# Kernel optimization log

Measured on AMD Instinct MI355X. Metric: run time of the kernel, lower is better.

Reference implementation:

```python
import jax, jax.numpy as jnp
import numpy as np

VOCAB = 64
EMB = 128
H = 256
OUT = 1
NUM_IN = 7
NUM_OUT = 4
B = 64
S = 2048
D_IN = EMB + NUM_OUT  # input_dim to the 1x1 convs


def setup_inputs() -> dict:
    key = jax.random.key(0)
    ks = jax.random.split(key, 12)
    ev = jax.random.randint(ks[0], (B, S, 1), 0, VOCAB).astype(jnp.float32)
    num = jax.random.normal(ks[1], (B, S, NUM_IN), dtype=jnp.float32)
    X = jnp.concatenate([ev, num], axis=-1)  # [B,S,1+NUM_IN]
    sc = lambda fan_in: 1.0 / np.sqrt(fan_in)
    return {
        "X": X,
        "emb": jax.random.normal(ks[2], (VOCAB, EMB), dtype=jnp.float32),
        "num_W": jax.random.normal(ks[3], (NUM_IN, NUM_OUT), dtype=jnp.float32) * sc(NUM_IN),
        "num_b": jnp.zeros((NUM_OUT,), jnp.float32),
        "Wf": jax.random.normal(ks[4], (D_IN, 3 * H), dtype=jnp.float32) * sc(D_IN),
        "bf": jnp.zeros((3 * H,), jnp.float32),
        "Wb": jax.random.normal(ks[5], (D_IN, 3 * H), dtype=jnp.float32) * sc(D_IN),
        "bb": jnp.zeros((3 * H,), jnp.float32),
        "Mu": jax.random.normal(ks[6], (2 * H, 1), dtype=jnp.float32) * sc(2 * H),
        "out_W": jax.random.normal(ks[7], (2 * H, OUT), dtype=jnp.float32) * sc(2 * H),
        "out_b": jnp.zeros((OUT,), jnp.float32),
    }


def _fo_pool(conv_out):
    # conv_out: [B, S, 3H] (already time-ordered as desired). Returns [B, S, H]
    Z, F, O = jnp.split(conv_out, 3, axis=-1)  # O computed but unused (as in source)
    Z = jnp.tanh(Z)
    F = jax.nn.sigmoid(F)
    # scan over time with state [B, H]
    Zt = jnp.swapaxes(Z, 0, 1)  # [S,B,H]
    Ft = jnp.swapaxes(F, 0, 1)
    h0 = jnp.zeros(Z.shape[::2][:1] + Z.shape[2:], Z.dtype) if False else jnp.zeros((Z.shape[0], Z.shape[2]), Z.dtype)
    def step(h, zf):
        z, f = zf
        h = f * h + (1.0 - f) * z
        return h, h
    _, hs = jax.lax.scan(step, h0, (Zt, Ft))  # [S,B,H] in scan order
    return jnp.swapaxes(hs, 0, 1)  # [B,S,H]


def reference(X, emb, num_W, num_b, Wf, bf, Wb, bb, Mu, out_W, out_b):
    ev = X[:, :, 0].astype(jnp.int32)            # event ids
    num = X[:, :, 1:]                             # numeric features [B,S,7]
    e = emb[ev]                                   # [B,S,EMB]
    n = num @ num_W + num_b                       # [B,S,NUM_OUT]
    x = jnp.concatenate([e, n], axis=-1)          # [B,S,D_IN]
    cf = x @ Wf + bf                              # 1x1 conv == pointwise linear, [B,S,3H]
    cb = x @ Wb + bb
    h_fwd = _fo_pool(cf)                          # [B,S,H], time order
    # backward direction: source iterates t = S-1..0 and stacks in append order
    h_bwd = _fo_pool(cb[:, ::-1, :])              # [B,S,H], reversed-time order (faithful)
    hc = jnp.concatenate([h_fwd, h_bwd], axis=-1) # [B,S,2H]
    scores = hc @ Mu                              # [B,S,1]
    w = jax.nn.softmax(scores, axis=1)
    ctx = jnp.sum(hc * w, axis=1)                 # [B,2H]
    return ctx @ out_W + out_b                    # [B,OUT]
```

## Files before the change

kernel.cpp:

```cpp
#include <hip/hip_runtime.h>
#include <stdint.h>

#define VOCABN 64
#define EMBN   128
#define HDIM   256
#define NUMIN  7
#define BN     64
#define SN     2048
#define TWOH   512
#define SEG    16
#define SEGLEN 128

#define CZ 2.8853900818f
#define CF 1.4426950409f

__device__ __forceinline__ float rcpf(float x){ return __builtin_amdgcn_rcpf(x); }

__device__ __forceinline__ float fast_exp2(float x){
#if __has_builtin(__builtin_amdgcn_exp2f)
    return __builtin_amdgcn_exp2f(x);
#else
    return exp2f(x);
#endif
}

__device__ __forceinline__ float2 pk_fma_s_lo(uint64_t a, float2 b, float2 c){
    float2 d;
    asm("v_pk_fma_f32 %0, %1, %2, %3 op_sel_hi:[0,1,1]" : "=v"(d) : "s"(a), "v"(b), "v"(c));
    return d;
}
__device__ __forceinline__ float2 pk_fma_s_hi(uint64_t a, float2 b, float2 c){
    float2 d;
    asm("v_pk_fma_f32 %0, %1, %2, %3 op_sel:[1,0,0] op_sel_hi:[1,1,1]" : "=v"(d) : "s"(a), "v"(b), "v"(c));
    return d;
}

__device__ __forceinline__ uint32_t cvt_pk_bf16(float a, float b){
    uint32_t r;
    asm("v_cvt_pk_bf16_f32 %0, %1, %2" : "=v"(r) : "v"(a), "v"(b));
    return r;
}

__device__ __forceinline__ float waveRedDpp(float x){
    x += __int_as_float(__builtin_amdgcn_update_dpp(0, __float_as_int(x), 0x111, 0xf, 0xf, false));
    x += __int_as_float(__builtin_amdgcn_update_dpp(0, __float_as_int(x), 0x112, 0xf, 0xf, false));
    x += __int_as_float(__builtin_amdgcn_update_dpp(0, __float_as_int(x), 0x114, 0xf, 0xf, false));
    x += __int_as_float(__builtin_amdgcn_update_dpp(0, __float_as_int(x), 0x118, 0xf, 0xf, false));
    x += __int_as_float(__builtin_amdgcn_update_dpp(0, __float_as_int(x), 0x142, 0xa, 0xf, false));
    x += __int_as_float(__builtin_amdgcn_update_dpp(0, __float_as_int(x), 0x143, 0xc, 0xf, false));
    return x;
}

__global__ __launch_bounds__(256) void k0_prep(const float* __restrict__ X, float* __restrict__ Xp)
{
    const int r = blockIdx.x*256 + threadIdx.x;
    const float4* src = (const float4*)(X + (size_t)r*8);
    const float4 a = src[0], b4 = src[1];
    float4* dst = (float4*)(Xp + (size_t)r*8);
    dst[0] = make_float4(a.y, a.z, a.w, b4.x);
    dst[1] = make_float4(b4.y, b4.z, b4.w, __int_as_float((int)a.x * (HDIM*8)));
}

__global__ __launch_bounds__(512) void k1_tables(
    const float* __restrict__ emb, const float* __restrict__ num_W, const float* __restrict__ num_b,
    const float* __restrict__ Wf, const float* __restrict__ bf,
    const float* __restrict__ Wb, const float* __restrict__ bb,
    float* __restrict__ T, float* __restrict__ U)
{
    const int blk = blockIdx.x;
    const int c = threadIdx.x;
    const int j = c & (HDIM-1);
    const int g = c >> 8;
    const int col = g*HDIM + j;
    const float gs = g ? CF : CZ;
    if (blk < 2*VOCABN) {
        const int dir = blk & 1, v = blk >> 1;
        const float* W    = dir ? Wb : Wf;
        const float* bias = dir ? bb : bf;
        float acc = bias[col];
        const float* e = emb + (size_t)v*EMBN;
        #pragma unroll 8
        for (int k=0;k<EMBN;++k) acc = fmaf(e[k], W[(size_t)k*768 + col], acc);
        #pragma unroll
        for (int m=0;m<4;++m)    acc = fmaf(num_b[m], W[(size_t)(EMBN+m)*768 + col], acc);
        T[(((size_t)dir*VOCABN + v)*HDIM + j)*2 + g] = acc * gs;
    } else {
        const int dir = blk - 2*VOCABN;
        const float* W = dir ? Wb : Wf;
        #pragma unroll
        for (int i=0;i<NUMIN;++i){
            float acc = 0.f;
            #pragma unroll
            for (int m=0;m<4;++m) acc = fmaf(num_W[i*4+m], W[(size_t)(EMBN+m)*768 + col], acc);
            U[(((size_t)dir*8 + i)*HDIM + j)*2 + g] = acc * gs;
        }
    }
}

template<int MODE>
__global__ __launch_bounds__(128) void k2_scan(
    const float* __restrict__ Xp, const float* __restrict__ T, const float* __restrict__ U,
    const float* __restrict__ Mu, const float* __restrict__ w,
    const float* __restrict__ hstart,
    float* __restrict__ aArr, float* __restrict__ cArr,
    float* __restrict__ swp, float* __restrict__ ctxp, uint32_t* __restrict__ h2)
{
    const int bid = blockIdx.x;
    const int seg = bid & (SEG-1);
    const int dir = (bid >> 4) & 1;
    const int b   = bid >> 5;
    const int j   = threadIdx.x;
    const int blk = (b*2+dir)*SEG + seg;
    const size_t segIdx = (size_t)blk*HDIM + j;

    const float2* Td2 = (const float2*)T + (size_t)dir*VOCABN*HDIM;
    const float2* Ud2 = (const float2*)U + (size_t)dir*8*HDIM;
    float2 uLo0=Ud2[0*HDIM+j],     uLo1=Ud2[1*HDIM+j],     uLo2=Ud2[2*HDIM+j],
           uLo3=Ud2[3*HDIM+j],     uLo4=Ud2[4*HDIM+j],     uLo5=Ud2[5*HDIM+j],
           uLo6=Ud2[6*HDIM+j];
    float2 uHi0=Ud2[0*HDIM+j+128], uHi1=Ud2[1*HDIM+j+128], uHi2=Ud2[2*HDIM+j+128],
           uHi3=Ud2[3*HDIM+j+128], uHi4=Ud2[4*HDIM+j+128], uHi5=Ud2[5*HDIM+j+128],
           uHi6=Ud2[6*HDIM+j+128];
    const float muLo = (MODE==1 || MODE==3) ? Mu[dir*HDIM + j]       : 0.f;
    const float muHi = (MODE==1 || MODE==3) ? Mu[dir*HDIM + j + 128] : 0.f;

    const int sBeg = seg*SEGLEN;
    const int r0   = b*SN + (dir ? (SN-1-sBeg) : sBeg);
    const int dstep= dir ? -1 : 1;
    const uint64_t* xq = (const uint64_t*)Xp;
    const float* wb = w + (size_t)b*SN + sBeg;
    const char* Tb = (const char*)Td2;
    const int j8 = j*8;

    #define ROWQ(si,k) (xq[(size_t)(r0 + dstep*(si))*4 + (k)])
    #define TROW(q)    (Tb + (int)((q)>>32))

    uint64_t qa0=ROWQ(0,0), qa1=ROWQ(0,1), qa2=ROWQ(0,2), qa3=ROWQ(0,3);
    uint64_t qb0=ROWQ(1,0), qb1=ROWQ(1,1), qb2=ROWQ(1,2), qb3=ROWQ(1,3);
    uint64_t qc0=ROWQ(2,0), qc1=ROWQ(2,1), qc2=ROWQ(2,2), qc3=ROWQ(2,3);
    uint64_t qd0=ROWQ(3,0), qd1=ROWQ(3,1), qd2=ROWQ(3,2), qd3=ROWQ(3,3);
    const char* tp0 = TROW(qa3);
    const char* tp1 = TROW(qb3);
    float2 tLo0 = *(const float2*)(tp0 + j8);
    float2 tHi0 = *(const float2*)(tp0 + j8 + 1024);
    float2 tLo1 = *(const float2*)(tp1 + j8);
    float2 tHi1 = *(const float2*)(tp1 + j8 + 1024);

    float hLo = (MODE==0) ? 0.f : hstart[segIdx];
    float hHi = (MODE==0) ? 0.f : hstart[segIdx + 128];
    float aaccLo = 1.f, aaccHi = 1.f;
    float ctxLo = 0.f, ctxHi = 0.f;
    float hpLo = 0.f, hpHi = 0.f;
    float* swpp = swp + (size_t)(b*4 + dir*2 + (j>>6))*SN + sBeg;
    uint32_t* h2p = h2 + (size_t)blk*(SEGLEN/2)*HDIM + j;

    #pragma unroll 4
    for (int si=0; si<SEGLEN; ++si){
        const int i4 = (si+4 < SEGLEN) ? si+4 : SEGLEN-1;
        const uint64_t qe0=ROWQ(i4,0), qe1=ROWQ(i4,1), qe2=ROWQ(i4,2), qe3=ROWQ(i4,3);
        const char* tp2 = TROW(qc3);
        const float2 tLo2 = *(const float2*)(tp2 + j8);
        const float2 tHi2 = *(const float2*)(tp2 + j8 + 1024);

        float2 zfLo = tLo0, zfHi = tHi0;
        zfLo = pk_fma_s_lo(qa0, uLo0, zfLo);  zfHi = pk_fma_s_lo(qa0, uHi0, zfHi);
        zfLo = pk_fma_s_hi(qa0, uLo1, zfLo);  zfHi = pk_fma_s_hi(qa0, uHi1, zfHi);
        zfLo = pk_fma_s_lo(qa1, uLo2, zfLo);  zfHi = pk_fma_s_lo(qa1, uHi2, zfHi);
        zfLo = pk_fma_s_hi(qa1, uLo3, zfLo);  zfHi = pk_fma_s_hi(qa1, uHi3, zfHi);
        zfLo = pk_fma_s_lo(qa2, uLo4, zfLo);  zfHi = pk_fma_s_lo(qa2, uHi4, zfHi);
        zfLo = pk_fma_s_hi(qa2, uLo5, zfLo);  zfHi = pk_fma_s_hi(qa2, uHi5, zfHi);
        zfLo = pk_fma_s_lo(qa3, uLo6, zfLo);  zfHi = pk_fma_s_lo(qa3, uHi6, zfHi);

        const float e2zL = fast_exp2(zfLo.x), efL = fast_exp2(zfLo.y);
        const float e2zH = fast_exp2(zfHi.x), efH = fast_exp2(zfHi.y);
        const float a2L = 1.f + e2zL, a1L = 1.f + efL;
        const float a2H = 1.f + e2zH, a1H = 1.f + efH;
        const float rL = rcpf(a1L * a2L);
        const float rH = rcpf(a1H * a2H);
        hLo = fmaf(efL * hLo, a2L, e2zL - 1.f) * rL;
        hHi = fmaf(efH * hHi, a2H, e2zH - 1.f) * rH;

        if (MODE==0){
            aaccLo *= efL * a2L * rL;
            aaccHi *= efH * a2H * rH;
        } else if (MODE==1 || MODE==3){
            float pr = waveRedDpp(fmaf(hHi, muHi, hLo * muLo));
            if ((j & 63) == 63) swpp[si] = pr;
            if (MODE==1){
                if (si & 1){
                    h2p[0]   = cvt_pk_bf16(hpLo, hLo);
                    h2p[128] = cvt_pk_bf16(hpHi, hHi);
                    h2p += HDIM;
                } else { hpLo = hLo; hpHi = hHi; }
            }
        } else {
            const float ws_ = wb[si];
            ctxLo = fmaf(ws_, hLo, ctxLo);
            ctxHi = fmaf(ws_, hHi, ctxHi);
        }
        qa0=qb0; qa1=qb1; qa2=qb2; qa3=qb3;
        qb0=qc0; qb1=qc1; qb2=qc2; qb3=qc3;
        qc0=qd0; qc1=qd1; qc2=qd2; qc3=qd3;
        qd0=qe0; qd1=qe1; qd2=qe2; qd3=qe3;
        tLo0=tLo1; tHi0=tHi1; tLo1=tLo2; tHi1=tHi2;
    }
    #undef ROWQ
    #undef TROW
    if (MODE==0){
        aArr[segIdx] = aaccLo; aArr[segIdx+128] = aaccHi;
        cArr[segIdx] = hLo;    cArr[segIdx+128] = hHi;
    }
    if (MODE==2){ ctxp[segIdx] = ctxLo; ctxp[segIdx+128] = ctxHi; }
}

__global__ __launch_bounds__(256) void k_compose(const float* __restrict__ aArr, const float* __restrict__ cArr,
                                                 float* __restrict__ hstart)
{
    const int bd = blockIdx.x;
    const int j  = threadIdx.x;
    float h = 0.f;
    #pragma unroll
    for (int seg=0; seg<SEG; ++seg){
        const size_t idx = ((size_t)bd*SEG + seg)*HDIM + j;
        hstart[idx] = h;
        h = fmaf(aArr[idx], h, cArr[idx]);
    }
}

__global__ __launch_bounds__(256) void k3_softmax(const float* __restrict__ swp, float* __restrict__ w)
{
    __shared__ float sc[SN];
    __shared__ float red[4];
    const int b = blockIdx.x, t = threadIdx.x;
    for (int s=t; s<SN; s+=256){
        float acc = 0.f;
        #pragma unroll
        for (int r=0;r<4;++r) acc += swp[((size_t)b*4 + r)*SN + s];
        sc[s] = acc;
    }
    __syncthreads();
    float m = -3.4e38f;
    for (int s=t; s<SN; s+=256) m = fmaxf(m, sc[s]);
    #pragma unroll
    for (int o=32;o;o>>=1) m = fmaxf(m, __shfl_xor(m,o,64));
    if ((t&63)==0) red[t>>6] = m;
    __syncthreads();
    m = fmaxf(fmaxf(red[0],red[1]), fmaxf(red[2],red[3]));
    float zs = 0.f;
    for (int s=t; s<SN; s+=256){
        float e = __expf(sc[s]-m);
        sc[s] = e;
        zs += e;
    }
    #pragma unroll
    for (int o=32;o;o>>=1) zs += __shfl_xor(zs,o,64);
    __syncthreads();
    if ((t&63)==0) red[t>>6] = zs;
    __syncthreads();
    zs = red[0]+red[1]+red[2]+red[3];
    float invz = rcpf(zs);
    for (int s=t; s<SN; s+=256) w[(size_t)b*SN + s] = sc[s]*invz;
}

__global__ __launch_bounds__(256) void k4_ctx(const uint32_t* __restrict__ h2, const float* __restrict__ w,
                                              float* __restrict__ ctxp)
{
    const int bid = blockIdx.x;
    const int seg = bid & (SEG-1);
    const int dir = (bid >> 4) & 1;
    const int b   = bid >> 5;
    const int blk = (b*2+dir)*SEG + seg;
    const int j   = threadIdx.x;
    const float* wb = w + (size_t)b*SN + seg*SEGLEN;
    const uint32_t* hp = h2 + (size_t)blk*(SEGLEN/2)*HDIM + j;
    float acc = 0.f;
    #pragma unroll 8
    for (int si2=0; si2<SEGLEN/2; ++si2){
        const uint32_t pk = hp[(size_t)si2*HDIM];
        const float hlo = __int_as_float(pk << 16);
        const float hhi = __int_as_float(pk & 0xffff0000u);
        acc = fmaf(wb[2*si2  ], hlo, acc);
        acc = fmaf(wb[2*si2+1], hhi, acc);
    }
    ctxp[(size_t)blk*HDIM + j] = acc;
}

__global__ __launch_bounds__(512) void k5_out(const float* __restrict__ ctxp, const float* __restrict__ out_W,
                                              const float* __restrict__ out_b, float* __restrict__ out)
{
    __shared__ float red[8];
    const int b = blockIdx.x, c = threadIdx.x;
    const int dir = c >> 8, j = c & (HDIM-1);
    float acc = 0.f;
    #pragma unroll
    for (int seg=0; seg<SEG; ++seg)
        acc += ctxp[((size_t)(b*2+dir)*SEG + seg)*HDIM + j];
    float p = acc * out_W[c];
    #pragma unroll
    for (int o=32;o;o>>=1) p += __shfl_xor(p,o,64);
    if ((c&63)==0) red[c>>6] = p;
    __syncthreads();
    if (c==0){
        float t = 0.f;
        #pragma unroll
        for (int r=0;r<8;++r) t += red[r];
        out[b] = t + out_b[0];
    }
}

extern "C" void kernel_launch(void* const* d_in, const int* in_sizes, int n_in,
                              void* d_out, int out_size, void* d_ws, size_t ws_size,
                              hipStream_t stream)
{
    const float* X     = (const float*)d_in[0];
    const float* emb   = (const float*)d_in[1];
    const float* num_W = (const float*)d_in[2];
    const float* num_b = (const float*)d_in[3];
    const float* Wf    = (const float*)d_in[4];
    const float* bf    = (const float*)d_in[5];
    const float* Wb    = (const float*)d_in[6];
    const float* bb    = (const float*)d_in[7];
    const float* Mu    = (const float*)d_in[8];
    const float* out_W = (const float*)d_in[9];
    const float* out_b = (const float*)d_in[10];
    float* out = (float*)d_out;

    float* ws = (float*)d_ws;
    size_t off = 0;
    float* swp   = ws + off; off += (size_t)BN*4*SN;
    float* w     = ws + off; off += (size_t)BN*SN;
    float* T     = ws + off; off += (size_t)2*VOCABN*TWOH;
    float* U     = ws + off; off += (size_t)2*8*TWOH;
    float* aArr  = ws + off; off += (size_t)BN*2*SEG*HDIM;
    float* cArr  = ws + off; off += (size_t)BN*2*SEG*HDIM;
    float* hstart= ws + off; off += (size_t)BN*2*SEG*HDIM;
    float* ctxp  = ws + off; off += (size_t)BN*2*SEG*HDIM;
    float* Xp    = ws + off; off += (size_t)BN*SN*8;
    uint32_t* h2 = (uint32_t*)(ws + off);
    off += (size_t)BN*2*SEG*(SEGLEN/2)*HDIM;
    const bool useStore = ((size_t)off * sizeof(float)) <= ws_size;

    hipLaunchKernelGGL(k0_prep,     dim3(BN*SN/256),   dim3(256), 0, stream, X, Xp);
    hipLaunchKernelGGL(k1_tables,   dim3(2*VOCABN+2),  dim3(512), 0, stream,
                       emb, num_W, num_b, Wf, bf, Wb, bb, T, U);
    hipLaunchKernelGGL(k2_scan<0>,  dim3(BN*2*SEG),    dim3(128), 0, stream,
                       Xp, T, U, Mu, w, hstart, aArr, cArr, swp, ctxp, h2);
    hipLaunchKernelGGL(k_compose,   dim3(BN*2),        dim3(256), 0, stream,
                       aArr, cArr, hstart);
    if (useStore) {
        hipLaunchKernelGGL(k2_scan<1>, dim3(BN*2*SEG), dim3(128), 0, stream,
                           Xp, T, U, Mu, w, hstart, aArr, cArr, swp, ctxp, h2);
        hipLaunchKernelGGL(k3_softmax, dim3(BN),       dim3(256), 0, stream, swp, w);
        hipLaunchKernelGGL(k4_ctx,     dim3(BN*2*SEG), dim3(256), 0, stream, h2, w, ctxp);
    } else {
        hipLaunchKernelGGL(k2_scan<3>, dim3(BN*2*SEG), dim3(128), 0, stream,
                           Xp, T, U, Mu, w, hstart, aArr, cArr, swp, ctxp, h2);
        hipLaunchKernelGGL(k3_softmax, dim3(BN),       dim3(256), 0, stream, swp, w);
        hipLaunchKernelGGL(k2_scan<2>, dim3(BN*2*SEG), dim3(128), 0, stream,
                           Xp, T, U, Mu, w, hstart, aArr, cArr, swp, ctxp, h2);
    }
    hipLaunchKernelGGL(k5_out,      dim3(BN),          dim3(512), 0, stream,
                       ctxp, out_W, out_b, out);
}
```

Baseline: 160.8 us.

## Double scan segments and load X rows through vector registers

Splits each sequence into 32 segments of 64 steps instead of 16 of 128, which doubles the number of scan blocks and halves the serial chain per block. The per-row X data is now loaded as float4 vector loads into VGPRs, using a zero VGPR offset to force vector addressing, instead of scalar 64-bit loads feeding SGPR packed-FMA operands. A launch-bounds occupancy hint is added. In exchange, the compose pass has more segments to chain, and it is not visible whether the elided compose and softmax code was updated consistently.

New measurement: 215.3 us. 1.34x slower.

```diff
diff --git a/kernel.cpp b/kernel.cpp
--- a/kernel.cpp
+++ b/kernel.cpp
@@ -8,8 +8,8 @@
 #define BN     64
 #define SN     2048
 #define TWOH   512
-#define SEG    16
-#define SEGLEN 128
+#define SEG    32
+#define SEGLEN 64
 
 #define CZ 2.8853900818f
 #define CF 1.4426950409f
@@ -24,14 +24,14 @@
 #endif
 }
 
-__device__ __forceinline__ float2 pk_fma_s_lo(uint64_t a, float2 b, float2 c){
+__device__ __forceinline__ float2 pk_fma_blo(float2 a, float2 b, float2 c){
     float2 d;
-    asm("v_pk_fma_f32 %0, %1, %2, %3 op_sel_hi:[0,1,1]" : "=v"(d) : "s"(a), "v"(b), "v"(c));
+    asm("v_pk_fma_f32 %0, %1, %2, %3 op_sel_hi:[0,1,1]" : "=v"(d) : "v"(a), "v"(b), "v"(c));
     return d;
 }
-__device__ __forceinline__ float2 pk_fma_s_hi(uint64_t a, float2 b, float2 c){
+__device__ __forceinline__ float2 pk_fma_bhi(float2 a, float2 b, float2 c){
     float2 d;
-    asm("v_pk_fma_f32 %0, %1, %2, %3 op_sel:[1,0,0] op_sel_hi:[1,1,1]" : "=v"(d) : "s"(a), "v"(b), "v"(c));
+    asm("v_pk_fma_f32 %0, %1, %2, %3 op_sel:[1,0,0] op_sel_hi:[1,1,1]" : "=v"(d) : "v"(a), "v"(b), "v"(c));
     return d;
 }
 
@@ -49,6 +49,16 @@
     x += __int_as_float(__builtin_amdgcn_update_dpp(0, __float_as_int(x), 0x142, 0xa, 0xf, false));
     x += __int_as_float(__builtin_amdgcn_update_dpp(0, __float_as_int(x), 0x143, 0xc, 0xf, false));
     return x;
+}
+
+struct XRow { float2 p01, p23, p45, p6e; };
+__device__ __forceinline__ XRow loadRow(const float* p){
+    XRow r;
+    const float4 a = *(const float4*)p;
+    const float4 b = *(const float4*)(p + 4);
+    r.p01 = make_float2(a.x, a.y); r.p23 = make_float2(a.z, a.w);
+    r.p45 = make_float2(b.x, b.y); r.p6e = make_float2(b.z, b.w);
+    return r;
 }
 
 __global__ __launch_bounds__(256) void k0_prep(const float* __restrict__ X, float* __restrict__ Xp)
@@ -98,7 +108,7 @@
 }
 
 template<int MODE>
-__global__ __launch_bounds__(128) void k2_scan(
+__global__ __launch_bounds__(128, 4) void k2_scan(
     const float* __restrict__ Xp, const float* __restrict__ T, const float* __restrict__ U,
     const float* __restrict__ Mu, const float* __restrict__ w,
     const float* __restrict__ hstart,
@@ -107,8 +117,8 @@
 {
     const int bid = blockIdx.x;
     const int seg = bid & (SEG-1);
-    const int dir = (bid >> 4) & 1;
-    const int b   = bid >> 5;
+    const int dir = (bid >> 5) & 1;
+    const int b   = bid >> 6;
     const int j   = threadIdx.x;
     const int blk = (b*2+dir)*SEG + seg;
     const size_t segIdx = (size_t)blk*HDIM + j;
@@ -127,24 +137,27 @@
     const int sBeg = seg*SEGLEN;
     const int r0   = b*SN + (dir ? (SN-1-sBeg) : sBeg);
     const int dstep= dir ? -1 : 1;
-    const uint64_t* xq = (const uint64_t*)Xp;
-    const float* wb = w + (size_t)b*SN + sBeg;
+
+    int zv = 0;
+    asm("" : "+v"(zv));
+    const float* xrBase = Xp + (size_t)r0*8 + zv;
+    const float* wbv    = w + (size_t)b*SN + sBeg + zv;
     const char* Tb = (const char*)Td2;
     const int j8 = j*8;
 
-    #define ROWQ(si,k) (xq[(size_t)(r0 + dstep*(si))*4 + (k)])
-    #define TROW(q)    (Tb + (int)((q)>>32))
-
-    uint64_t qa0=ROWQ(0,0), qa1=ROWQ(0,1), qa2=ROWQ(0,2), qa3=ROWQ(0,3);
-    uint64_t qb0=ROWQ(1,0), qb1=ROWQ(1,1), qb2=ROWQ(1,2), qb3=ROWQ(1,3);
-    uint64_t qc0=ROWQ(2,0), qc1=ROWQ(2,1), qc2=ROWQ(2,2), qc3=ROWQ(2,3);
-    uint64_t qd0=ROWQ(3,0), qd1=ROWQ(3,1), qd2=ROWQ(3,2), qd3=ROWQ(3,3);
-    const char* tp0 = TROW(qa3);
-    const char* tp1 = TROW(qb3);
-    float2 tLo0 = *(const float2*)(tp0 + j8);
-    float2 tHi0 = *(const float2*)(tp0 + j8 + 1024);
-    float2 tLo1 = *(const float2*)(tp1 + j8);
-    float2 tHi1 = *(const float2*)(tp1 + j8 + 1024);
+    #define XROWP(si) (xrBase + (ptrdiff_t)(dstep*(si))*8)
+    #define EVOF(r)   __float_as_int((r).p6e.y)
+
+    XRow x0 = loadRow(XROWP(0));
+    XRow x1 = loadRow(XROWP(1));
+    XRow x2 = loadRow(XROWP(2));
+    XRow x3 = loadRow(XROWP(3));
+    const char* tp0 = Tb + (uint32_t)(EVOF(x0) + j8);
+    const char* tp1 = Tb + (uint32_t)(EVOF(x1) + j8);
+    float2 tLo0 = *(const float2*)tp0;
+    float2 tHi0 = *(const float2*)(tp0 + 1024);
+    float2 tLo1 = *(const float2*)tp1;
+    float2 tHi1 = *(const float2*)(tp1 + 1024);
 
     float hLo = (MODE==0) ? 0.f : hstart[segIdx];
     float hHi = (MODE==0) ? 0.f : hstart[segIdx + 128];
@@ -157,19 +170,19 @@
     #pragma unroll 4
     for (int si=0; si<SEGLEN; ++si){
         const int i4 = (si+4 < SEGLEN) ? si+4 : SEGLEN-1;
-        const uint64_t qe0=ROWQ(i4,0), qe1=ROWQ(i4,1), qe2=ROWQ(i4,2), qe3=ROWQ(i4,3);
-        const char* tp2 = TROW(qc3);
-        const float2 tLo2 = *(const float2*)(tp2 + j8);
-        const float2 tHi2 = *(const float2*)(tp2 + j8 + 1024);
+        const XRow x4 = loadRow(XROWP(i4));
+        const char* tp2 = Tb + (uint32_t)(EVOF(x2) + j8);
+        const float2 tLo2 = *(const float2*)tp2;
+        const float2 tHi2 = *(const float2*)(tp2 + 1024);
 
         float2 zfLo = tLo0, zfHi = tHi0;
-        zfLo = pk_fma_s_lo(qa0, uLo0, zfLo);  zfHi = pk_fma_s_lo(qa0, uHi0, zfHi);
-        zfLo = pk_fma_s_hi(qa0, uLo1, zfLo);  zfHi = pk_fma_s_hi(qa0, uHi1, zfHi);
-        zfLo = pk_fma_s_lo(qa1, uLo2, zfLo);  zfHi = pk_fma_s_lo(qa1, uHi2, zfHi);
-        zfLo = pk_fma_s_hi(qa1, uLo3, zfLo);  zfHi = pk_fma_s_hi(qa1, uHi3, zfHi);
-        zfLo = pk_fma_s_lo(qa2, uLo4, zfLo);  zfHi = pk_fma_s_lo(qa2, uHi4, zfHi);
-        zfLo = pk_fma_s_hi(qa2, uLo5, zfLo);  zfHi = pk_fma_s_hi(qa2, uHi5, zfHi);
-        zfLo = pk_fma_s_lo(qa3, uLo6, zfLo);  zfHi = pk_fma_s_lo(qa3, uHi6, zfHi);
+        zfLo = pk_fma_blo(x0.p01, uLo0, zfLo);  zfHi = pk_fma_blo(x0.p01, uHi0, zfHi);
+        zfLo = pk_fma_bhi(x0.p01, uLo1, zfLo);  zfHi = pk_fma_bhi(x0.p01, uHi1, zfHi);
+        zfLo = pk_fma_blo(x0.p23, uLo2, zfLo);  zfHi = pk_fma_blo(x0.p23, uHi2, zfHi);
+        zfLo = pk_fma_bhi(x0.p23, uLo3, zfLo);  zfHi = pk_fma_bhi(x0.p23, uHi3, zfHi);
+        zfLo = pk_fma_blo(x0.p45, uLo4, zfLo);  zfHi = pk_fma_blo(x0.p45, uHi4, zfHi);
+        zfLo = pk_fma_bhi(x0.p45, uLo5, zfLo);  zfHi = pk_fma_bhi(x0.p45, uHi5, zfHi);
+        zfLo = pk_fma_blo(x0.p6e, uLo6, zfLo);  zfHi = pk_fma_blo(x0.p6e, uHi6, zfHi);
 
         const float e2zL = fast_exp2(zfLo.x), efL = fast_exp2(zfLo.y);
         const float e2zH = fast_exp2(zfHi.x), efH = fast_exp2(zfHi.y);
@@ -194,18 +207,15 @@
                 } else { hpLo = hLo; hpHi = hHi; }
             }
         } else {
-            const float ws_ = wb[si];
+            const float ws_ = wbv[si];
             ctxLo = fmaf(ws_, hLo, ctxLo);
             ctxHi = fmaf(ws_, hHi, ctxHi);
         }
-        qa0=qb0; qa1=qb1; qa2=qb2; qa3=qb3;
-        qb0=qc0; qb1=qc1; qb2=qc2; qb3=qc3;
-        qc0=qd0; qc1=qd1; qc2=qd2; qc3=qd3;
-        qd0=qe0; qd1=qe1; qd2=qe2; qd3=qe3;
+        x0=x1; x1=x2; x2=x3; x3=x4;
         tLo0=tLo1; tHi0=tHi1; tLo1=tLo2; tHi1=tHi2;
     }
-    #undef ROWQ
-    #undef TROW
+    #undef XROWP
+    #undef EVOF
     if (MODE==0){
         aArr[segIdx] = aaccLo; aArr[segIdx+128] = aaccHi;
         cArr[segIdx] = hLo;    cArr[segIdx+128] = hHi;
@@ -267,8 +277,8 @@
 {
     const int bid = blockIdx.x;
     const int seg = bid & (SEG-1);
-    const int dir = (bid >> 4) & 1;
-    const int b   = bid >> 5;
+    const int dir = (bid >> 5) & 1;
+    const int b   = bid >> 6;
     const int blk = (b*2+dir)*SEG + seg;
     const int j   = threadIdx.x;
     const float* wb = w + (size_t)b*SN + seg*SEGLEN;
```
